# Performance work log

Hardware: AMD Instinct MI355X
Metric: run time of the kernel (lower is better)

Reference implementation:

```python
import jax, jax.numpy as jnp
import numpy as np

HID = 1024
INTER = 4096
NUM_EXPERTS = 4096
NUM_KEYS = 64  # floor(sqrt(4096))
TOP_K = 8
B, S = 2, 2048


def setup_inputs() -> dict:
    key = jax.random.key(0)
    ks = jax.random.split(key, 7)
    sc = 0.02
    return {
        "hidden_states": jax.random.normal(ks[0], (B, S, HID), jnp.float32),
        "w_gate": jax.random.normal(ks[1], (INTER, HID), jnp.float32) * sc,
        "w_up": jax.random.normal(ks[2], (INTER, HID), jnp.float32) * sc,
        "w_down": jax.random.normal(ks[3], (HID, INTER), jnp.float32) * sc,
        "w_router": jax.random.normal(ks[4], (NUM_KEYS * 2, HID), jnp.float32) * sc,
        "down_embed": jax.random.normal(ks[5], (NUM_EXPERTS, HID), jnp.float32) * sc,
        "up_embed": jax.random.normal(ks[6], (NUM_EXPERTS, HID), jnp.float32) * sc,
    }


def reference(hidden_states, w_gate, w_up, w_down, w_router, down_embed, up_embed):
    b, s, h = hidden_states.shape
    n = b * s
    # router: [b,s,2*nk] -> row-major reshape to (2, n, nk), matching torch .view
    router_logits = (hidden_states @ w_router.T).reshape(2, n, NUM_KEYS)
    # topk with k == nk is a full descending sort (faithful to torch .topk)
    scores_xy, idx_xy = jax.lax.top_k(router_logits, NUM_KEYS)
    scores_x, scores_y = scores_xy[0], scores_xy[1]  # (n, nk) each
    idx_x, idx_y = idx_xy[0], idx_xy[1]
    all_scores = (scores_x[:, :, None] + scores_y[:, None, :]).reshape(n, NUM_KEYS * NUM_KEYS)
    all_indices = (idx_x[:, :, None] * NUM_KEYS + idx_y[:, None, :]).reshape(n, NUM_KEYS * NUM_KEYS)
    scores, pos = jax.lax.top_k(all_scores, TOP_K)  # (n, top_k)
    indices = jnp.take_along_axis(all_indices, pos, axis=-1)
    routing_weights = jax.nn.softmax(scores, axis=-1)
    routing_weights = routing_weights / routing_weights.sum(-1, keepdims=True)  # norm_topk_prob
    de = down_embed[indices]  # (n, top_k, h)
    ue = up_embed[indices]    # (n, top_k, h)
    x_flat = hidden_states.reshape(n, h)
    ew = jnp.einsum('nkh,nh->nk', de, x_flat)
    ew = jax.nn.silu(ew) * routing_weights
    experts_states = jnp.einsum('nk,nkh->nh', ew, ue).reshape(b, s, h)
    mlp = (jax.nn.silu(x_flat @ w_gate.T) * (x_flat @ w_up.T)) @ w_down.T
    out = mlp.reshape(b, s, h) + experts_states
    return (out, router_logits)
```

## Files before the change

### kernel.cpp

```cpp
#include <hip/hip_runtime.h>
#include <hip/hip_bf16.h>
#include <stdint.h>

typedef __bf16 bf16;
typedef __attribute__((ext_vector_type(8))) __bf16 bf16x8;
typedef __attribute__((ext_vector_type(4))) float f32x4;

static constexpr int kTok = 4096;
static constexpr int kHid = 1024;
static constexpr int kInter = 4096;

#define GLDS16(g, l)                                                \
  __builtin_amdgcn_global_load_lds(                                 \
      (const __attribute__((address_space(1))) void*)(g),           \
      (__attribute__((address_space(3))) void*)(l), 16, 0, 0)

__global__ void __launch_bounds__(256) k_cvt_all(
    const float* X, const float* Wg, const float* Wu, const float* Wd,
    bf16* Xb, bf16* Wgb, bf16* Wub, bf16* Wdb) {
  const long i = ((long)blockIdx.x * 256 + threadIdx.x) * 8;
  const float* src;
  bf16* dst;
  switch (blockIdx.y) {
    case 0: src = X;  dst = Xb;  break;
    case 1: src = Wg; dst = Wgb; break;
    case 2: src = Wu; dst = Wub; break;
    default: src = Wd; dst = Wdb; break;
  }
  const f32x4 a = *(const f32x4*)(src + i);
  const f32x4 b = *(const f32x4*)(src + i + 4);
  bf16x8 o;
#pragma unroll
  for (int k = 0; k < 4; ++k) { o[k] = (bf16)a[k]; o[4 + k] = (bf16)b[k]; }
  *(bf16x8*)(dst + i) = o;
}

__global__ void __launch_bounds__(256, 2) gemm_gu_rt(
    const bf16* X, const bf16* Wg, const bf16* Wu,
    const float* Xf, const float* Wr, bf16* H, float* out1) {
  __shared__ bf16 smem[12288];
  const int t = threadIdx.x;
  const int w = t >> 6;
  const int L = t & 63;
  const int la = L & 15;
  const int lk = (L >> 4) * 8;
  const f32x4 fzero = {0.f, 0.f, 0.f, 0.f};

  if (blockIdx.x == 32) {
    bf16* sA = smem;
    bf16* sB = smem + 4096;
    const long m0 = (long)blockIdx.y * 128;
    const int wm = (w >> 1) * 64;
    const int wn = (w & 1) * 64;
    f32x4 acc[4][4];
#pragma unroll
    for (int i = 0; i < 4; ++i)
#pragma unroll
      for (int j = 0; j < 4; ++j) acc[i][j] = fzero;

    const int c0 = t, c1 = t + 256;
    const long ar0 = m0 + (c0 >> 2), ar1 = m0 + (c1 >> 2);
    const long br0 = (c0 >> 2), br1 = (c1 >> 2);
    const int ko = (c0 & 3) * 8;
    const bf16* sAr = sA + (wm + la) * 32 + lk;
    const bf16* sBr = sB + (wn + la) * 32 + lk;

    for (int kt = 0; kt < 32; ++kt) {
      const long k0 = (long)kt << 5;
      bf16x8 av0, av1, bv0, bv1;
      {
        const f32x4 x0 = *(const f32x4*)(Xf + ar0 * kHid + k0 + ko);
        const f32x4 x1 = *(const f32x4*)(Xf + ar0 * kHid + k0 + ko + 4);
        const f32x4 y0 = *(const f32x4*)(Xf + ar1 * kHid + k0 + ko);
        const f32x4 y1 = *(const f32x4*)(Xf + ar1 * kHid + k0 + ko + 4);
        const f32x4 p0 = *(const f32x4*)(Wr + br0 * kHid + k0 + ko);
        const f32x4 p1 = *(const f32x4*)(Wr + br0 * kHid + k0 + ko + 4);
        const f32x4 q0 = *(const f32x4*)(Wr + br1 * kHid + k0 + ko);
        const f32x4 q1 = *(const f32x4*)(Wr + br1 * kHid + k0 + ko + 4);
#pragma unroll
        for (int i = 0; i < 4; ++i) {
          av0[i] = (bf16)x0[i]; av0[4 + i] = (bf16)x1[i];
          av1[i] = (bf16)y0[i]; av1[4 + i] = (bf16)y1[i];
          bv0[i] = (bf16)p0[i]; bv0[4 + i] = (bf16)p1[i];
          bv1[i] = (bf16)q0[i]; bv1[4 + i] = (bf16)q1[i];
        }
      }
      __syncthreads();
      *(bf16x8*)(sA + c0 * 8) = av0;
      *(bf16x8*)(sA + c1 * 8) = av1;
      *(bf16x8*)(sB + c0 * 8) = bv0;
      *(bf16x8*)(sB + c1 * 8) = bv1;
      __syncthreads();
      bf16x8 af[4], bfm[4];
#pragma unroll
      for (int i = 0; i < 4; ++i) {
        af[i] = *(const bf16x8*)(sAr + i * 512);
        bfm[i] = *(const bf16x8*)(sBr + i * 512);
      }
#pragma unroll
      for (int i = 0; i < 4; ++i)
#pragma unroll
        for (int j = 0; j < 4; ++j)
          acc[i][j] = __builtin_amdgcn_mfma_f32_16x16x32_bf16(
              af[i], bfm[j], acc[i][j], 0, 0, 0);
    }
    const long col0 = wn + la;
    const long row0 = m0 + wm + (L >> 4) * 4;
#pragma unroll
    for (int i = 0; i < 4; ++i)
#pragma unroll
      for (int j = 0; j < 4; ++j)
#pragma unroll
        for (int r = 0; r < 4; ++r)
          out1[(row0 + i * 16 + r) * 128 + col0 + j * 16] = acc[i][j][r];
    return;
  }

  bf16* sX = smem;
  bf16* sG = smem + 4096;
  bf16* sU = smem + 8192;
  const long m0 = (long)blockIdx.y * 128;
  const long n0 = (long)blockIdx.x * 128;
  const int wm = (w >> 1) * 64;
  const int wn = (w & 1) * 64;

  f32x4 accG[4][4], accU[4][4];
#pragma unroll
  for (int i = 0; i < 4; ++i)
#pragma unroll
    for (int j = 0; j < 4; ++j) { accG[i][j] = fzero; accU[i][j] = fzero; }

  const int r0 = t >> 2;
  const int ko = (t & 3) * 8;
  const bf16* gX0 = X + (m0 + r0) * kHid + ko;
  const bf16* gX1 = gX0 + (long)64 * kHid;
  const bf16* gG0 = Wg + (n0 + r0) * kHid + ko;
  const bf16* gG1 = gG0 + (long)64 * kHid;
  const bf16* gU0 = Wu + (n0 + r0) * kHid + ko;
  const bf16* gU1 = gU0 + (long)64 * kHid;
  bf16* lX0 = sX + w * 512;
  bf16* lX1 = sX + 2048 + w * 512;
  bf16* lG0 = sG + w * 512;
  bf16* lG1 = sG + 2048 + w * 512;
  bf16* lU0 = sU + w * 512;
  bf16* lU1 = sU + 2048 + w * 512;

  const bf16* sXr = sX + (wm + la) * 32 + lk;
  const bf16* sGr = sG + (wn + la) * 32 + lk;
  const bf16* sUr = sU + (wn + la) * 32 + lk;

  for (int kt = 0; kt < kHid / 32; ++kt) {
    const long k0 = (long)kt << 5;
    GLDS16(gX0 + k0, lX0);
    GLDS16(gX1 + k0, lX1);
    GLDS16(gG0 + k0, lG0);
    GLDS16(gG1 + k0, lG1);
    GLDS16(gU0 + k0, lU0);
    GLDS16(gU1 + k0, lU1);
    __syncthreads();
    bf16x8 af[4], bg[4], bu[4];
#pragma unroll
    for (int i = 0; i < 4; ++i) {
      af[i] = *(const bf16x8*)(sXr + i * 512);
      bg[i] = *(const bf16x8*)(sGr + i * 512);
      bu[i] = *(const bf16x8*)(sUr + i * 512);
    }
#pragma unroll
    for (int i = 0; i < 4; ++i)
#pragma unroll
      for (int j = 0; j < 4; ++j) {
        accG[i][j] = __builtin_amdgcn_mfma_f32_16x16x32_bf16(af[i], bg[j],
                                                             accG[i][j], 0, 0, 0);
        accU[i][j] = __builtin_amdgcn_mfma_f32_16x16x32_bf16(af[i], bu[j],
                                                             accU[i][j], 0, 0, 0);
      }
    __syncthreads();
  }
  const long col0 = n0 + wn + la;
  const long row0 = m0 + wm + (L >> 4) * 4;
#pragma unroll
  for (int i = 0; i < 4; ++i)
#pragma unroll
    for (int j = 0; j < 4; ++j)
#pragma unroll
      for (int r = 0; r < 4; ++r) {
        const float g = accG[i][j][r];
        const float u = accU[i][j][r];
        H[(row0 + i * 16 + r) * kInter + col0 + j * 16] =
            (bf16)(g / (1.f + __expf(-g)) * u);
      }
}

__global__ void __launch_bounds__(256, 2) gemm_down(
    const bf16* Hs, const bf16* Wd, float* out0, float* p1) {
  constexpr int K = kInter, N = kHid;
  __shared__ bf16 sA[128 * 32];
  __shared__ bf16 sB[128 * 32];
  const int t = threadIdx.x;
  const int w = t >> 6;
  const int L = t & 63;
  const long m0 = (long)blockIdx.y * 128;
  const long n0 = (long)blockIdx.x * 128;
  const long zb = (long)blockIdx.z * 2048;
  const int wm = (w >> 1) * 64;
  const int wn = (w & 1) * 64;

  f32x4 acc[4][4];
  const f32x4 fzero = {0.f, 0.f, 0.f, 0.f};
#pragma unroll
  for (int i = 0; i < 4; ++i)
#pragma unroll
    for (int j = 0; j < 4; ++j) acc[i][j] = fzero;

  const int r0 = t >> 2;
  const int ko = (t & 3) * 8;
  const bf16* gA0 = Hs + (m0 + r0) * K + zb + ko;
  const bf16* gA1 = gA0 + (long)64 * K;
  const bf16* gB0 = Wd + (n0 + r0) * K + zb + ko;
  const bf16* gB1 = gB0 + (long)64 * K;
  bf16* lA0 = sA + w * 512;
  bf16* lA1 = sA + 2048 + w * 512;
  bf16* lB0 = sB + w * 512;
  bf16* lB1 = sB + 2048 + w * 512;

  const int la = L & 15;
  const int lk = (L >> 4) * 8;
  const bf16* sAr = sA + (wm + la) * 32 + lk;
  const bf16* sBr = sB + (wn + la) * 32 + lk;

  for (int kt = 0; kt < 64; ++kt) {
    const long k0 = (long)kt << 5;
    GLDS16(gA0 + k0, lA0);
    GLDS16(gA1 + k0, lA1);
    GLDS16(gB0 + k0, lB0);
    GLDS16(gB1 + k0, lB1);
    __syncthreads();
    bf16x8 af[4], bfm[4];
#pragma unroll
    for (int i = 0; i < 4; ++i) {
      af[i] = *(const bf16x8*)(sAr + i * 512);
      bfm[i] = *(const bf16x8*)(sBr + i * 512);
    }
#pragma unroll
    for (int i = 0; i < 4; ++i)
#pragma unroll
      for (int j = 0; j < 4; ++j)
        acc[i][j] = __builtin_amdgcn_mfma_f32_16x16x32_bf16(af[i], bfm[j],
                                                            acc[i][j], 0, 0, 0);
    __syncthreads();
  }
  float* dst = (blockIdx.z == 0) ? out0 : p1;
  const long col0 = n0 + wn + la;
  const long row0 = m0 + wm + (L >> 4) * 4;
#pragma unroll
  for (int i = 0; i < 4; ++i)
#pragma unroll
    for (int j = 0; j < 4; ++j)
#pragma unroll
      for (int r = 0; r < 4; ++r)
        dst[(row0 + i * 16 + r) * N + col0 + j * 16] = acc[i][j][r];
}

__global__ void __launch_bounds__(256) route_expert(
    const float* logits, const float* X, const float* dE, const float* uE,
    const float* p1, float* out0) {
  __shared__ float s_vals[4][128];
  __shared__ int s_idx[4][128];
  const int w = threadIdx.x >> 6;
  const int L = threadIdx.x & 63;
  const int j = blockIdx.x * 4 + w;

  const int half = (j & 1) * 64;
  const int rx = j >> 1;
  const float vx = logits[(long)rx * 128 + half + L];
  const float vy = logits[(long)(2048 + rx) * 128 + half + L];

  int rkx = 0, rky = 0;
  for (int m = 0; m < 64; ++m) {
    const float mx = __shfl(vx, m);
    const float my = __shfl(vy, m);
    rkx += (mx > vx) || (mx == vx && m < L);
    rky += (my > vy) || (my == vy && m < L);
  }
  rkx &= 63;
  rky &= 63;
  s_vals[w][rkx] = vx;
  s_idx[w][rkx] = L;
  s_vals[w][64 + rky] = vy;
  s_idx[w][64 + rky] = L;
  __syncthreads();

  int p = 0, q = 0;
  const bool valid = (L < 20);
  if (L < 8)       { p = L;      q = 0; }
  else if (L < 12) { p = L - 8;  q = 1; }
  else if (L < 14) { p = L - 12; q = 2; }
  else if (L < 16) { p = L - 14; q = 3; }
  else if (L < 20) { p = 0;      q = L - 12; }
  const float kNegBig = -3.0e38f;
  float myv = valid ? (s_vals[w][p] + s_vals[w][64 + q]) : kNegBig;
  int mypos = valid ? (p * 64 + q) : 0x7fffffff;

  float topv[8];
  int tope[8];
#pragma unroll
  for (int r = 0; r < 8; ++r) {
    float bv = myv;
    int bp = mypos;
#pragma unroll
    for (int d = 32; d > 0; d >>= 1) {
      const float ov = __shfl_xor(bv, d);
      const int op = __shfl_xor(bp, d);
      if (ov > bv || (ov == bv && op < bp)) { bv = ov; bp = op; }
    }
    topv[r] = bv;
    const int pp = (bp >> 6) & 127, qq = bp & 63;
    tope[r] = (s_idx[w][pp] * 64 + s_idx[w][64 + qq]) & 4095;
    if (mypos == bp) myv = kNegBig;
  }

  float e[8], wsum = 0.f;
#pragma unroll
  for (int r = 0; r < 8; ++r) {
    e[r] = __expf(topv[r] - topv[0]);
    wsum += e[r];
  }
  const float winv = 1.f / wsum;

  const long xoff = (long)j * kHid + L * 16;
  float xv[16], acc[16];
#pragma unroll
  for (int v4 = 0; v4 < 4; ++v4) {
    const f32x4 xl = *(const f32x4*)(X + xoff + v4 * 4);
#pragma unroll
    for (int i = 0; i < 4; ++i) { xv[v4 * 4 + i] = xl[i]; acc[v4 * 4 + i] = 0.f; }
  }

  for (int r = 0; r < 8; ++r) {
    const long eo = (long)tope[r] * kHid + L * 16;
    float d = 0.f;
#pragma unroll
    for (int v4 = 0; v4 < 4; ++v4) {
      const f32x4 dl = *(const f32x4*)(dE + eo + v4 * 4);
#pragma unroll
      for (int i = 0; i < 4; ++i) d += dl[i] * xv[v4 * 4 + i];
    }
#pragma unroll
    for (int dd = 32; dd > 0; dd >>= 1) d += __shfl_xor(d, dd);
    const float ew = d / (1.f + __expf(-d)) * (e[r] * winv);
#pragma unroll
    for (int v4 = 0; v4 < 4; ++v4) {
      const f32x4 ul = *(const f32x4*)(uE + eo + v4 * 4);
#pragma unroll
      for (int i = 0; i < 4; ++i) acc[v4 * 4 + i] += ew * ul[i];
    }
  }

  float* po = out0 + xoff;
  const float* pp1 = p1 + xoff;
#pragma unroll
  for (int v4 = 0; v4 < 4; ++v4) {
    f32x4 ov = *(const f32x4*)(po + v4 * 4);
    const f32x4 pv = *(const f32x4*)(pp1 + v4 * 4);
#pragma unroll
    for (int i = 0; i < 4; ++i) ov[i] += pv[i] + acc[v4 * 4 + i];
    *(f32x4*)(po + v4 * 4) = ov;
  }
}

extern "C" void kernel_launch(void* const* d_in, const int* in_sizes, int n_in,
                              void* d_out, int out_size, void* d_ws,
                              size_t ws_size, hipStream_t stream) {
  (void)in_sizes; (void)n_in; (void)out_size; (void)ws_size;
  const float* X  = (const float*)d_in[0];
  const float* Wg = (const float*)d_in[1];
  const float* Wu = (const float*)d_in[2];
  const float* Wd = (const float*)d_in[3];
  const float* Wr = (const float*)d_in[4];
  const float* dE = (const float*)d_in[5];
  const float* uE = (const float*)d_in[6];

  float* out0 = (float*)d_out;
  float* out1 = out0 + (size_t)kTok * kHid;

  bf16* wsH = (bf16*)d_ws;
  bf16* Xb  = wsH + (size_t)kTok * kInter;
  bf16* Wgb = Xb  + (size_t)kTok * kHid;
  bf16* Wub = Wgb + (size_t)kInter * kHid;
  bf16* Wdb = Wub + (size_t)kInter * kHid;
  float* p1 = (float*)Xb;

  dim3 blk(256);
  k_cvt_all<<<dim3(2048, 4), blk, 0, stream>>>(X, Wg, Wu, Wd,
                                               Xb, Wgb, Wub, Wdb);
  gemm_gu_rt<<<dim3(33, 32), blk, 0, stream>>>(Xb, Wgb, Wub, X, Wr, wsH, out1);
  gemm_down<<<dim3(8, 32, 2), blk, 0, stream>>>(wsH, Wdb, out0, p1);
  route_expert<<<dim3(kTok / 4), blk, 0, stream>>>(out1, X, dE, uE, p1, out0);
}
```

Measured before the change: 379.3 us.

## Fuse routed-expert work into down GEMM launch and drop split-K

The down-projection GEMM no longer splits K across two z-slices. It runs as 256 blocks, each doing the full K=4096, inside a combined 1280-block launch whose remaining 1024 blocks do the routing and expert computation concurrently, writing to a scratch buffer. A small elementwise kernel then adds the expert result into the output. The gate/up grid is transposed so the router blocks sit in the last y row. The aim is to overlap the bandwidth-bound expert gather with the MFMA GEMM and cut one partial-sum pass. The cost is longer per-block GEMM work (64 K-steps over fewer blocks) and an extra launch.

After: 389.3 us. 1.03x slower.

```diff
diff --git a/kernel.cpp b/kernel.cpp
--- a/kernel.cpp
+++ b/kernel.cpp
@@ -46,10 +46,10 @@
   const int lk = (L >> 4) * 8;
   const f32x4 fzero = {0.f, 0.f, 0.f, 0.f};
 
-  if (blockIdx.x == 32) {
+  if (blockIdx.y == 32) {
     bf16* sA = smem;
     bf16* sB = smem + 4096;
-    const long m0 = (long)blockIdx.y * 128;
+    const long m0 = (long)blockIdx.x * 128;
     const int wm = (w >> 1) * 64;
     const int wn = (w & 1) * 64;
     f32x4 acc[4][4];
@@ -191,84 +191,84 @@
       }
 }
 
-__global__ void __launch_bounds__(256, 2) gemm_down(
-    const bf16* Hs, const bf16* Wd, float* out0, float* p1) {
-  constexpr int K = kInter, N = kHid;
-  __shared__ bf16 sA[128 * 32];
-  __shared__ bf16 sB[128 * 32];
+__global__ void __launch_bounds__(256, 2) gemm_down_re(
+    const bf16* Hs, const bf16* Wd, const float* logits, const float* Xf,
+    const float* dE, const float* uE, float* out0, float* e0) {
+  __shared__ char smem[16384];
+  const int bid = blockIdx.x;
   const int t = threadIdx.x;
   const int w = t >> 6;
   const int L = t & 63;
-  const long m0 = (long)blockIdx.y * 128;
-  const long n0 = (long)blockIdx.x * 128;
-  const long zb = (long)blockIdx.z * 2048;
-  const int wm = (w >> 1) * 64;
-  const int wn = (w & 1) * 64;
-
-  f32x4 acc[4][4];
-  const f32x4 fzero = {0.f, 0.f, 0.f, 0.f};
-#pragma unroll
-  for (int i = 0; i < 4; ++i)
-#pragma unroll
-    for (int j = 0; j < 4; ++j) acc[i][j] = fzero;
-
-  const int r0 = t >> 2;
-  const int ko = (t & 3) * 8;
-  const bf16* gA0 = Hs + (m0 + r0) * K + zb + ko;
-  const bf16* gA1 = gA0 + (long)64 * K;
-  const bf16* gB0 = Wd + (n0 + r0) * K + zb + ko;
-  const bf16* gB1 = gB0 + (long)64 * K;
-  bf16* lA0 = sA + w * 512;
-  bf16* lA1 = sA + 2048 + w * 512;
-  bf16* lB0 = sB + w * 512;
-  bf16* lB1 = sB + 2048 + w * 512;
-
-  const int la = L & 15;
-  const int lk = (L >> 4) * 8;
-  const bf16* sAr = sA + (wm + la) * 32 + lk;
-  const bf16* sBr = sB + (wn + la) * 32 + lk;
-
-  for (int kt = 0; kt < 64; ++kt) {
-    const long k0 = (long)kt << 5;
-    GLDS16(gA0 + k0, lA0);
-    GLDS16(gA1 + k0, lA1);
-    GLDS16(gB0 + k0, lB0);
-    GLDS16(gB1 + k0, lB1);
-    __syncthreads();
-    bf16x8 af[4], bfm[4];
-#pragma unroll
-    for (int i = 0; i < 4; ++i) {
-      af[i] = *(const bf16x8*)(sAr + i * 512);
-      bfm[i] = *(const bf16x8*)(sBr + i * 512);
-    }
+
+  if (bid < 256) {
+    constexpr int K = kInter, N = kHid;
+    bf16* sA = (bf16*)smem;
+    bf16* sB = (bf16*)smem + 4096;
+    const int bx = bid & 7;
+    const int by = bid >> 3;
+    const long m0 = (long)by * 128;
+    const long n0 = (long)bx * 128;
+    const int wm = (w >> 1) * 64;
+    const int wn = (w & 1) * 64;
+    const int la = L & 15;
+    const int lk = (L >> 4) * 8;
+
+    f32x4 acc[4][4];
+    const f32x4 fzero = {0.f, 0.f, 0.f, 0.f};
 #pragma unroll
     for (int i = 0; i < 4; ++i)
 #pragma unroll
+      for (int j = 0; j < 4; ++j) acc[i][j] = fzero;
+
+    const int r0 = t >> 2;
+    const int ko = (t & 3) * 8;
+    const bf16* gA0 = Hs + (m0 + r0) * K + ko;
+    const bf16* gA1 = gA0 + (long)64 * K;
+    const bf16* gB0 = Wd + (n0 + r0) * K + ko;
+    const bf16* gB1 = gB0 + (long)64 * K;
+    bf16* lA0 = sA + w * 512;
+    bf16* lA1 = sA + 2048 + w * 512;
+    bf16* lB0 = sB + w * 512;
+    bf16* lB1 = sB + 2048 + w * 512;
+    const bf16* sAr = sA + (wm + la) * 32 + lk;
+    const bf16* sBr = sB + (wn + la) * 32 + lk;
+
+    for (int kt = 0; kt < K / 32; ++kt) {
+      const long k0 = (long)kt << 5;
+      GLDS16(gA0 + k0, lA0);
+      GLDS16(gA1 + k0, lA1);
+      GLDS16(gB0 + k0, lB0);
+      GLDS16(gB1 + k0, lB1);
+      __syncthreads();
+      bf16x8 af[4], bfm[4];
+#pragma unroll
+      for (int i = 0; i < 4; ++i) {
+        af[i] = *(const bf16x8*)(sAr + i * 512);
+        bfm[i] = *(const bf16x8*)(sBr + i * 512);
+      }
+#pragma unroll
+      for (int i = 0; i < 4; ++i)
+#pragma unroll
+        for (int j = 0; j < 4; ++j)
+          acc[i][j] = __builtin_amdgcn_mfma_f32_16x16x32_bf16(
+              af[i], bfm[j], acc[i][j], 0, 0, 0);
+      __syncthreads();
+    }
+    const long col0 = n0 + wn + la;
+    const long row0 = m0 + wm + (L >> 4) * 4;
+#pragma unroll
+    for (int i = 0; i < 4; ++i)
+#pragma unroll
       for (int j = 0; j < 4; ++j)
-        acc[i][j] = __builtin_amdgcn_mfma_f32_16x16x32_bf16(af[i], bfm[j],
-                                                            acc[i][j], 0, 0, 0);
-    __syncthreads();
-  }
-  float* dst = (blockIdx.z == 0) ? out0 : p1;
-  const long col0 = n0 + wn + la;
-  const long row0 = m0 + wm + (L >> 4) * 4;
-#pragma unroll
-  for (int i = 0; i < 4; ++i)
-#pragma unroll
-    for (int j = 0; j < 4; ++j)
-#pragma unroll
-      for (int r = 0; r < 4; ++r)
-        dst[(row0 + i * 16 + r) * N + col0 + j * 16] = acc[i][j][r];
-}
-
-__global__ void __launch_bounds__(256) route_expert(
-    const float* logits, const float* X, const float* dE, const float* uE,
-    const float* p1, float* out0) {
-  __shared__ float s_vals[4][128];
-  __shared__ int s_idx[4][128];
-  const int w = threadIdx.x >> 6;
-  const int L = threadIdx.x & 63;
-  const int j = blockIdx.x * 4 + w;
+#pragma unroll
+        for (int r = 0; r < 4; ++r)
+          out0[(row0 + i * 16 + r) * N + col0 + j * 16] = acc[i][j][r];
+    return;
+  }
+
+  float (*s_vals)[128] = (float (*)[128])smem;
+  int (*s_idx)[128] = (int (*)[128])(smem + 2048);
+  const int j = (bid - 256) * 4 + w;
 
   const int half = (j & 1) * 64;
   const int rx = j >> 1;
@@ -331,7 +331,7 @@
   float xv[16], acc[16];
 #pragma unroll
   for (int v4 = 0; v4 < 4; ++v4) {
-    const f32x4 xl = *(const f32x4*)(X + xoff + v4 * 4);
+    const f32x4 xl = *(const f32x4*)(Xf + xoff + v4 * 4);
 #pragma unroll
     for (int i = 0; i < 4; ++i) { xv[v4 * 4 + i] = xl[i]; acc[v4 * 4 + i] = 0.f; }
   }
@@ -356,16 +356,26 @@
     }
   }
 
-  float* po = out0 + xoff;
-  const float* pp1 = p1 + xoff;
+  float* pe = e0 + xoff;
 #pragma unroll
   for (int v4 = 0; v4 < 4; ++v4) {
-    f32x4 ov = *(const f32x4*)(po + v4 * 4);
-    const f32x4 pv = *(const f32x4*)(pp1 + v4 * 4);
-#pragma unroll
-    for (int i = 0; i < 4; ++i) ov[i] += pv[i] + acc[v4 * 4 + i];
-    *(f32x4*)(po + v4 * 4) = ov;
-  }
+    f32x4 ov;
+#pragma unroll
+    for (int i = 0; i < 4; ++i) ov[i] = acc[v4 * 4 + i];
+    *(f32x4*)(pe + v4 * 4) = ov;
+  }
+}
+
+__global__ void __launch_bounds__(256) k_add(float* out0, const float* e0) {
+  const long i = ((long)blockIdx.x * 256 + threadIdx.x) * 8;
+  f32x4 a0 = *(const f32x4*)(out0 + i);
+  f32x4 a1 = *(const f32x4*)(out0 + i + 4);
+  const f32x4 b0 = *(const f32x4*)(e0 + i);
+  const f32x4 b1 = *(const f32x4*)(e0 + i + 4);
+#pragma unroll
+  for (int k = 0; k < 4; ++k) { a0[k] += b0[k]; a1[k] += b1[k]; }
+  *(f32x4*)(out0 + i) = a0;
+  *(f32x4*)(out0 + i + 4) = a1;
 }
 
 extern "C" void kernel_launch(void* const* d_in, const int* in_sizes, int n_in,
@@ -388,12 +398,13 @@
   bf16* Wgb = Xb  + (size_t)kTok * kHid;
   bf16* Wub = Wgb + (size_t)kInter * kHid;
   bf16* Wdb = Wub + (size_t)kInter * kHid;
-  float* p1 = (float*)Xb;
+  float* e0 = (float*)Xb;
 
   dim3 blk(256);
   k_cvt_all<<<dim3(2048, 4), blk, 0, stream>>>(X, Wg, Wu, Wd,
                                                Xb, Wgb, Wub, Wdb);
-  gemm_gu_rt<<<dim3(33, 32), blk, 0, stream>>>(Xb, Wgb, Wub, X, Wr, wsH, out1);
-  gemm_down<<<dim3(8, 32, 2), blk, 0, stream>>>(wsH, Wdb, out0, p1);
-  route_expert<<<dim3(kTok / 4), blk, 0, stream>>>(out1, X, dE, uE, p1, out0);
+  gemm_gu_rt<<<dim3(32, 33), blk, 0, stream>>>(Xb, Wgb, Wub, X, Wr, wsH, out1);
+  gemm_down_re<<<dim3(1280), blk, 0, stream>>>(wsH, Wdb, out1, X, dE, uE,
+                                               out0, e0);
+  k_add<<<dim3(2048), blk, 0, stream>>>(out0, e0);
 }
```
